# Performance work log

Measured on AMD Instinct MI355X. Metric: run time of the kernel, lower is better.

## Reference

```python
import jax, jax.numpy as jnp
import numpy as np

R = 8          # gate_r
SIGMA = 4.0
PER_SPK_MAX = 32
TOP_M = 64
N_HEADS = 8


def _window_mean(A, spikes, r):
    # A:[B,T], spikes:[B,S] int -> mean of A over [ti-r, ti+r] clipped to [0,T)
    B, T = A.shape
    off = jnp.arange(-r, r + 1)
    t = spikes[:, :, None] + off                      # [B,S,W]
    valid = (t >= 0) & (t < T)
    tc = jnp.clip(t, 0, T - 1)
    vals = A[jnp.arange(B)[:, None, None], tc]        # [B,S,W]
    return (vals * valid).sum(-1) / jnp.maximum(valid.sum(-1), 1)


def setup_inputs() -> dict:
    key = jax.random.key(0)
    ks = jax.random.split(key, 12)
    Kspk, B, T, S0 = 3, 8, 8192, 128
    d_proj = d_c = d_model = 512
    s = 0.02
    return {
        'proj_feats': jax.random.normal(ks[0], (B, T, d_proj), jnp.float32),
        'h_ctc': jax.random.normal(ks[1], (Kspk, B, T, d_c), jnp.float32),
        'A': jax.random.uniform(ks[2], (Kspk, B, T), jnp.float32),
        'spikes': jax.random.randint(ks[3], (Kspk, B, S0), 0, T),
        'W_mem': jax.random.normal(ks[4], (d_proj, d_model), jnp.float32) * s,
        'b_mem': jnp.zeros((d_model,), jnp.float32),
        'W_kv': jax.random.normal(ks[5], (Kspk, d_c, 2 * d_model), jnp.float32) * s,
        'b_kv': jnp.zeros((Kspk, 2 * d_model), jnp.float32),
        'W_q': jax.random.normal(ks[6], (d_model, d_model), jnp.float32) * s,
        'b_q': jnp.zeros((d_model,), jnp.float32),
        'W_qkv': jax.random.normal(ks[7], (d_model, 3 * d_model), jnp.float32) * s,
        'b_qkv': jnp.zeros((3 * d_model,), jnp.float32),
        'W_attn_out': jax.random.normal(ks[8], (d_model, d_model), jnp.float32) * s,
        'b_attn_out': jnp.zeros((d_model,), jnp.float32),
        'W_o': jax.random.normal(ks[9], (d_model, d_model), jnp.float32) * s,
        'b_o': jnp.zeros((d_model,), jnp.float32),
    }


def reference(proj_feats, h_ctc, A, spikes, W_mem, b_mem, W_kv, b_kv,
              W_q, b_q, W_qkv, b_qkv, W_attn_out, b_attn_out, W_o, b_o):
    Kspk, B, T, _ = h_ctc.shape
    d_model = W_mem.shape[1]
    hd = d_model // N_HEADS
    # memory = projected mixed features (K = V = M_mem)
    M = proj_feats @ W_mem + b_mem                                  # [B,T,d]
    Wqh, Wkh, Wvh = jnp.split(W_qkv, 3, axis=1)
    bqh, bkh, bvh = jnp.split(b_qkv, 3)
    k_mem = (M @ Wkh + bkh).reshape(B, T, N_HEADS, hd)
    v_mem = (M @ Wvh + bvh).reshape(B, T, N_HEADS, hd)
    off = jnp.arange(-R, R + 1)
    gauss = jnp.exp(-0.5 * (off / SIGMA) ** 2)                      # [W]
    bidx = jnp.arange(B)[:, None, None]
    tracks = []
    for k in range(Kspk):
        A_k, sp = A[k], spikes[k]
        k_keep = min(PER_SPK_MAX, sp.shape[1], TOP_M)
        # prune spikes by local mean of A (top-k per batch)
        sc = jnp.where((sp >= 0) & (sp < T), _window_mean(A_k, sp, R), -1e9)
        _, top_idx = jax.lax.top_k(sc, k_keep)
        spk = jnp.take_along_axis(sp, top_idx, axis=1)              # [B,S]
        # Gaussian-weighted window pooling around each kept spike
        t = spk[:, :, None] + off                                   # [B,S,W]
        valid = (t >= 0) & (t < T)
        tc = jnp.clip(t, 0, T - 1)
        w = gauss * A_k[bidx, tc] * valid                           # [B,S,W]
        Z = jnp.einsum('bsw,bswd->bsd', w, h_ctc[k][bidx, tc]) / (w.sum(-1, keepdims=True) + 1e-6)
        vmask = ((spk >= 0) & (spk < T)).astype(M.dtype)            # all ones here
        # K_seed = first half of kv_ctc[k](Z); queries
        K_seed = (Z @ W_kv[k] + b_kv[k])[..., :d_model]
        Qk = jnp.tanh(K_seed @ W_q + b_q)                           # [B,S,d]
        # cross-attention (nn.MultiheadAttention, batch_first)
        q = (Qk @ Wqh + bqh).reshape(B, -1, N_HEADS, hd)
        attn = jax.nn.softmax(
            jnp.einsum('bqhd,bthd->bhqt', q, k_mem) / jnp.sqrt(jnp.float32(hd)), axis=-1)
        ctx = jnp.einsum('bhqt,bthd->bqhd', attn, v_mem).reshape(B, -1, d_model)
        fused = (ctx @ W_attn_out + b_attn_out) @ W_o + b_o
        # confidence gate (computed under no_grad in the original)
        conf = jax.lax.stop_gradient(jnp.where(vmask > 0, _window_mean(A_k, spk, R), 0.0))
        gk = jax.nn.sigmoid(2.0 * conf) * vmask
        tracks.append(fused * gk[..., None])
    return jnp.concatenate(tracks, axis=1)                          # [B, K*S, d]
```

## Files before the change

kernel.cpp:

```cpp
#include <hip/hip_runtime.h>
#include <hip/hip_bf16.h>


#define T_LEN 8192
#define DMODEL 512
#define NROWS 768

typedef __hip_bfloat16 bf16;
typedef short s16x8 __attribute__((ext_vector_type(8)));
typedef float f32x4 __attribute__((ext_vector_type(4)));
typedef float f4 __attribute__((ext_vector_type(4)));
typedef float f2 __attribute__((ext_vector_type(2)));
typedef int i32x4 __attribute__((ext_vector_type(4)));
typedef struct __attribute__((aligned(16))) { bf16 v[8]; } bf8;

__global__ __launch_bounds__(256) void prep_w2t(const float* __restrict__ Wmem,
                                                const float* __restrict__ Wqkv,
                                                bf16* __restrict__ w2t) {
  __shared__ __align__(16) float As[16][68];
  __shared__ __align__(16) float Bs[16][68];
  int tid = threadIdx.x;
  int j0 = blockIdx.x * 64, i0 = blockIdx.y * 64;
  int ty = tid >> 4, tx = tid & 15;
  float c[4][4];
#pragma unroll
  for (int a = 0; a < 4; a++)
#pragma unroll
    for (int b = 0; b < 4; b++) c[a][b] = 0.f;

  for (int l0 = 0; l0 < 512; l0 += 16) {
    __syncthreads();
    {
      int l = tid >> 4, j4 = (tid & 15) * 4;
      f4 v = *(const f4*)&Wqkv[(size_t)(l0 + l) * 1536 + 512 + j0 + j4];
      *(f4*)&As[l][j4] = v;
    }
    {
      int i = tid >> 2, l4 = (tid & 3) * 4;
      f4 v = *(const f4*)&Wmem[(size_t)(i0 + i) * 512 + l0 + l4];
      Bs[l4 + 0][i] = v[0];
      Bs[l4 + 1][i] = v[1];
      Bs[l4 + 2][i] = v[2];
      Bs[l4 + 3][i] = v[3];
    }
    __syncthreads();
#pragma unroll
    for (int l = 0; l < 16; l++) {
      f4 a = *(f4*)&As[l][ty * 4];
      f4 b = *(f4*)&Bs[l][tx * 4];
#pragma unroll
      for (int jj = 0; jj < 4; jj++)
#pragma unroll
        for (int ii = 0; ii < 4; ii++) c[jj][ii] += a[jj] * b[ii];
    }
  }
#pragma unroll
  for (int jj = 0; jj < 4; jj++)
#pragma unroll
    for (int ii = 0; ii < 4; ii++)
      w2t[(size_t)(j0 + ty * 4 + jj) * 512 + i0 + tx * 4 + ii] =
          __float2bfloat16(c[jj][ii]);
}

__global__ void bias2_kernel(const float* __restrict__ bmem,
                             const float* __restrict__ Wqkv,
                             const float* __restrict__ bqkv,
                             float* __restrict__ b2) {
  int j = blockIdx.x * 256 + threadIdx.x;
  float acc = bqkv[512 + j];
  for (int l = 0; l < 512; l++) acc += bmem[l] * Wqkv[(size_t)l * 1536 + 512 + j];
  b2[j] = acc;
}

__global__ __launch_bounds__(256) void cvt_bf16(const float* __restrict__ x,
                                                bf16* __restrict__ y) {
  int i = blockIdx.x * 256 + threadIdx.x;
  const f4* p = (const f4*)x;
  f4 a = p[(size_t)i * 2], b = p[(size_t)i * 2 + 1];
  __align__(16) bf16 o[8];
  o[0] = __float2bfloat16(a[0]);
  o[1] = __float2bfloat16(a[1]);
  o[2] = __float2bfloat16(a[2]);
  o[3] = __float2bfloat16(a[3]);
  o[4] = __float2bfloat16(b[0]);
  o[5] = __float2bfloat16(b[1]);
  o[6] = __float2bfloat16(b[2]);
  o[7] = __float2bfloat16(b[3]);
  ((f4*)y)[i] = *(f4*)o;
}

__global__ __launch_bounds__(256) void kv_gemm(const bf16* __restrict__ A,
                                               const bf16* __restrict__ Bt,
                                               const float* __restrict__ bias,
                                               bf16* __restrict__ C) {
  __shared__ __align__(16) bf16 As[128 * 32];
  __shared__ __align__(16) bf16 Bs[128 * 32];
  int tid = threadIdx.x;
  int lane = tid & 63, wave = tid >> 6;
  int wm = wave & 1, wn = wave >> 1;
  int m0 = blockIdx.y * 128, n0 = blockIdx.x * 128;
  int l15 = lane & 15, lq = lane >> 4;
  f32x4 acc[4][4];
#pragma unroll
  for (int mi = 0; mi < 4; mi++)
#pragma unroll
    for (int ni = 0; ni < 4; ni++) acc[mi][ni] = (f32x4){0.f, 0.f, 0.f, 0.f};

  for (int k0 = 0; k0 < 512; k0 += 32) {
    __syncthreads();
#pragma unroll
    for (int t = 0; t < 2; t++) {
      int c = t * 256 + tid;
      int row = c >> 2, kq = c & 3;
      s16x8 av = *(const s16x8*)&A[(size_t)(m0 + row) * 512 + k0 + kq * 8];
      s16x8 bv = *(const s16x8*)&Bt[(size_t)(n0 + row) * 512 + k0 + kq * 8];
      *(s16x8*)&As[c * 8] = av;
      *(s16x8*)&Bs[c * 8] = bv;
    }
    __syncthreads();
    s16x8 af[4], bfr[4];
#pragma unroll
    for (int mi = 0; mi < 4; mi++)
      af[mi] = *(s16x8*)&As[(wm * 64 + mi * 16 + l15) * 32 + lq * 8];
#pragma unroll
    for (int ni = 0; ni < 4; ni++)
      bfr[ni] = *(s16x8*)&Bs[(wn * 64 + ni * 16 + l15) * 32 + lq * 8];
#pragma unroll
    for (int mi = 0; mi < 4; mi++)
#pragma unroll
      for (int ni = 0; ni < 4; ni++)
        acc[mi][ni] = __builtin_amdgcn_mfma_f32_16x16x32_bf16(af[mi], bfr[ni],
                                                              acc[mi][ni], 0, 0, 0);
  }
#pragma unroll
  for (int ni = 0; ni < 4; ni++) {
    int col = n0 + wn * 64 + ni * 16 + l15;
    float bcol = bias[col];
#pragma unroll
    for (int mi = 0; mi < 4; mi++) {
      int row = m0 + wm * 64 + mi * 16 + lq * 4;
      f32x4 v = acc[mi][ni];
#pragma unroll
      for (int r = 0; r < 4; r++)
        C[(size_t)(row + r) * 1024 + col] = __float2bfloat16(v[r] + bcol);
    }
  }
}

__global__ __launch_bounds__(128) void topk_kernel(const float* __restrict__ A,
                                                   const int* __restrict__ spikes,
                                                   int* __restrict__ spk_out,
                                                   float* __restrict__ w_out,
                                                   float* __restrict__ winv_out,
                                                   float* __restrict__ gk_out) {
  int kb = blockIdx.x;
  int i = threadIdx.x;
  const float* Ab = A + (size_t)kb * T_LEN;
  __shared__ float s_sc[128];
  __shared__ int s_sp[128];
  __shared__ int s_sel[32];
  int t0 = spikes[kb * 128 + i];
  s_sp[i] = t0;
  float sum = 0.f;
  int cnt = 0;
#pragma unroll
  for (int o = -8; o <= 8; o++) {
    int t = t0 + o;
    if (t >= 0 && t < T_LEN) { sum += Ab[t]; cnt++; }
  }
  float sc = (t0 >= 0 && t0 < T_LEN) ? (sum / (float)max(cnt, 1)) : -1e9f;
  s_sc[i] = sc;
  __syncthreads();
  float sci = s_sc[i];
  int rank = 0;
  for (int j = 0; j < 128; j++) {
    float scj = s_sc[j];
    if (scj > sci || (scj == sci && j < i)) rank++;
  }
  if (rank < 32) s_sel[rank] = i;
  __syncthreads();
  if (i < 32) {
    int sel = s_sel[i];
    int spkv = s_sp[sel];
    float conf = s_sc[sel];
    int r = kb * 32 + i;
    spk_out[r] = spkv;
    bool vmask = (spkv >= 0 && spkv < T_LEN);
    float wsum = 0.f;
#pragma unroll
    for (int o = 0; o < 17; o++) {
      int t = spkv + o - 8;
      bool v = vmask && (t >= 0) && (t < T_LEN);
      int tc = min(max(t, 0), T_LEN - 1);
      float off = (float)(o - 8) * 0.25f;
      float g = expf(-0.5f * off * off);
      float wv = v ? g * Ab[tc] : 0.f;
      wsum += wv;
      w_out[r * 17 + o] = wv;
    }
    winv_out[r] = 1.f / (wsum + 1e-6f);
    gk_out[r] = vmask ? (1.f / (1.f + expf(-2.f * conf))) : 0.f;
  }
}

__global__ __launch_bounds__(256) void z_gather(const float* __restrict__ hctc,
                                                const int* __restrict__ spk,
                                                const float* __restrict__ warr,
                                                const float* __restrict__ winv,
                                                float* __restrict__ Z) {
  int r = blockIdx.x;
  int tid = threadIdx.x;
  int kb = r >> 5;
  const float* h = hctc + (size_t)kb * T_LEN * DMODEL;
  int sp = spk[r];
  float wi = winv[r];
  float acc0 = 0.f, acc1 = 0.f;
#pragma unroll
  for (int o = 0; o < 17; o++) {
    float wv = warr[r * 17 + o];
    int t = min(max(sp + o - 8, 0), T_LEN - 1);
    const float* hp = h + (size_t)t * DMODEL;
    acc0 += wv * hp[tid];
    acc1 += wv * hp[tid + 256];
  }
  Z[(size_t)r * DMODEL + tid] = acc0 * wi;
  Z[(size_t)r * DMODEL + tid + 256] = acc1 * wi;
}

__global__ __launch_bounds__(256) void seed_chain(
    const float* __restrict__ Z, const float* __restrict__ Wkv,
    const float* __restrict__ bkv, const float* __restrict__ Wq,
    const float* __restrict__ bq, const float* __restrict__ Wqkv,
    const float* __restrict__ bqkv, float* __restrict__ qout) {
  __shared__ float Zs[8][512];
  __shared__ float T1[8][512];
  __shared__ float T2[8][512];
  int tid = threadIdx.x;
  int r0 = blockIdx.x * 8;
  int k = r0 >> 8;
  for (int ii = 0; ii < 16; ii++) {
    int idx = tid + ii * 256;
    ((float*)Zs)[idx] = Z[(size_t)r0 * 512 + idx];
  }
  __syncthreads();
  int c0 = tid, c1 = tid + 256;
  {
    const float* W = Wkv + (size_t)k * 512 * 1024;
    float a0[8], a1[8];
#pragma unroll
    for (int i = 0; i < 8; i++) { a0[i] = 0.f; a1[i] = 0.f; }
#pragma unroll 4
    for (int l = 0; l < 512; l++) {
      float w0 = W[(size_t)l * 1024 + c0];
      float w1 = W[(size_t)l * 1024 + c1];
#pragma unroll
      for (int i = 0; i < 8; i++) {
        float z = Zs[i][l];
        a0[i] += z * w0;
        a1[i] += z * w1;
      }
    }
    float bb0 = bkv[k * 1024 + c0], bb1 = bkv[k * 1024 + c1];
#pragma unroll
    for (int i = 0; i < 8; i++) {
      T1[i][c0] = a0[i] + bb0;
      T1[i][c1] = a1[i] + bb1;
    }
  }
  __syncthreads();
  {
    float a0[8], a1[8];
#pragma unroll
    for (int i = 0; i < 8; i++) { a0[i] = 0.f; a1[i] = 0.f; }
#pragma unroll 4
    for (int l = 0; l < 512; l++) {
      float w0 = Wq[(size_t)l * 512 + c0];
      float w1 = Wq[(size_t)l * 512 + c1];
#pragma unroll
      for (int i = 0; i < 8; i++) {
        float z = T1[i][l];
        a0[i] += z * w0;
        a1[i] += z * w1;
      }
    }
    float bb0 = bq[c0], bb1 = bq[c1];
#pragma unroll
    for (int i = 0; i < 8; i++) {
      T2[i][c0] = tanhf(a0[i] + bb0);
      T2[i][c1] = tanhf(a1[i] + bb1);
    }
  }
  __syncthreads();
  {
    float a0[8], a1[8];
#pragma unroll
    for (int i = 0; i < 8; i++) { a0[i] = 0.f; a1[i] = 0.f; }
#pragma unroll 4
    for (int l = 0; l < 512; l++) {
      float w0 = Wqkv[(size_t)l * 1536 + c0];
      float w1 = Wqkv[(size_t)l * 1536 + c1];
#pragma unroll
      for (int i = 0; i < 8; i++) {
        float z = T2[i][l];
        a0[i] += z * w0;
        a1[i] += z * w1;
      }
    }
    float bb0 = bqkv[c0], bb1 = bqkv[c1];
#pragma unroll
    for (int i = 0; i < 8; i++) {
      qout[(size_t)(r0 + i) * 512 + c0] = a0[i] + bb0;
      qout[(size_t)(r0 + i) * 512 + c1] = a1[i] + bb1;
    }
  }
}


static __device__ __forceinline__ unsigned bf16rne(float f) {
  unsigned x = __builtin_bit_cast(unsigned, f);
  return (x + 0x7fffu + ((x >> 16) & 1u)) >> 16;
}
static __device__ __forceinline__ float bfval(unsigned u) {
  return __builtin_bit_cast(float, u << 16);
}
static __device__ __forceinline__ void hilo(float x, unsigned& h, unsigned& l) {
  h = bf16rne(x);
  l = bf16rne(x - bfval(h));
}

__global__ __launch_bounds__(256) void attn_kernel(const bf16* __restrict__ kv,
                                                   const float* __restrict__ qws,
                                                   float* __restrict__ pm,
                                                   float* __restrict__ pl,
                                                   float* __restrict__ pu) {
  __shared__ short Vts[4][2048];
  __shared__ float ctxc[4][32][68];
  __shared__ float cm[4][32];
  __shared__ float cl[4][32];

  int tid = threadIdx.x;
  int w = tid >> 6, lane = tid & 63;
  int l15 = lane & 15, g = lane >> 4;
  int bx = blockIdx.x;
  int c = bx & 7, h = (bx >> 3) & 7, b = (bx >> 6) & 7, k = bx >> 9;
  int kb = k * 8 + b;
  const short* kvS = (const short*)kv;
  int hoff = h * 64;
  int rowK = b * T_LEN + c * 1024 + w * 256;

  s16x8 qf[2][2][2];
#pragma unroll
  for (int qt = 0; qt < 2; qt++)
#pragma unroll
    for (int ds = 0; ds < 2; ds++) {
      const float* qp =
          qws + (size_t)(kb * 32 + qt * 16 + l15) * 512 + hoff + ds * 32 + g * 8;
      f4 x = *(const f4*)qp;
      f4 y = *(const f4*)(qp + 4);
      x *= 0.125f;
      y *= 0.125f;
      s16x8 hi, lo;
#pragma unroll
      for (int j = 0; j < 4; j++) {
        unsigned hb, lb;
        hilo(x[j], hb, lb);
        hi[j] = (short)hb;
        lo[j] = (short)lb;
        hilo(y[j], hb, lb);
        hi[4 + j] = (short)hb;
        lo[4 + j] = (short)lb;
      }
      qf[qt][ds][0] = hi;
      qf[qt][ds][1] = lo;
    }

  float mq[2] = {-3.0e38f, -3.0e38f};
  float lq[2] = {0.f, 0.f};
  f32x4 ctx[4][2];
#pragma unroll
  for (int dt = 0; dt < 4; dt++)
#pragma unroll
    for (int qt = 0; qt < 2; qt++) ctx[dt][qt] = (f32x4){0.f, 0.f, 0.f, 0.f};

  int a0 = (l15 + (((2 * g) & 3) << 4)) << 2;
  int a1 = a0 + 64;

  for (int st = 0; st < 8; st++) {
    int tbase = st * 32;
    s16x8 kf[2][2];
#pragma unroll
    for (int mt = 0; mt < 2; mt++) {
      size_t krow = (size_t)(rowK + tbase + mt * 16 + l15) * 1024 + hoff;
#pragma unroll
      for (int ds = 0; ds < 2; ds++)
        kf[mt][ds] = *(const s16x8*)(kvS + krow + ds * 32 + g * 8);
    }
    s16x8 vv[4];
#pragma unroll
    for (int i = 0; i < 4; i++)
      vv[i] = *(const s16x8*)(kvS +
                              (size_t)(rowK + tbase + i * 8 + (lane >> 3)) * 1024 +
                              512 + hoff + (lane & 7) * 8);
#pragma unroll
    for (int i = 0; i < 4; i++) {
      int kk = i * 8 + (lane >> 3);
      int dbase = (lane & 7) * 8;
#pragma unroll
      for (int j = 0; j < 8; j++) {
        int d = dbase + j;
        Vts[w][d * 32 + (kk & 7) + ((i ^ ((d >> 3) & 3)) << 3)] = vv[i][j];
      }
    }
    s16x8 vfr[4];
#pragma unroll
    for (int dt = 0; dt < 4; dt++) {
      int d = dt * 16 + l15;
      vfr[dt] = *(const s16x8*)&Vts[w][d * 32 + ((g ^ ((d >> 3) & 3)) << 3)];
    }
    f32x4 sa[2][2];
#pragma unroll
    for (int mt = 0; mt < 2; mt++)
#pragma unroll
      for (int qt = 0; qt < 2; qt++) {
        f32x4 acc = (f32x4){0.f, 0.f, 0.f, 0.f};
        acc = __builtin_amdgcn_mfma_f32_16x16x32_bf16(kf[mt][0], qf[qt][0][0], acc, 0, 0, 0);
        acc = __builtin_amdgcn_mfma_f32_16x16x32_bf16(kf[mt][0], qf[qt][0][1], acc, 0, 0, 0);
        acc = __builtin_amdgcn_mfma_f32_16x16x32_bf16(kf[mt][1], qf[qt][1][0], acc, 0, 0, 0);
        acc = __builtin_amdgcn_mfma_f32_16x16x32_bf16(kf[mt][1], qf[qt][1][1], acc, 0, 0, 0);
        sa[mt][qt] = acc;
      }
#pragma unroll
    for (int qt = 0; qt < 2; qt++) {
      f32x4 s0 = sa[0][qt], s1 = sa[1][qt];
      float tm = fmaxf(fmaxf(fmaxf(s0[0], s0[1]), fmaxf(s0[2], s0[3])),
                       fmaxf(fmaxf(s1[0], s1[1]), fmaxf(s1[2], s1[3])));
      tm = fmaxf(tm, __shfl_xor(tm, 16, 64));
      tm = fmaxf(tm, __shfl_xor(tm, 32, 64));
      float mn = fmaxf(mq[qt], tm);
      float p0[4], p1[4];
      float ps = 0.f;
#pragma unroll
      for (int j = 0; j < 4; j++) {
        p0[j] = __expf(s0[j] - mn);
        p1[j] = __expf(s1[j] - mn);
        ps += p0[j] + p1[j];
      }
      ps += __shfl_xor(ps, 16, 64);
      ps += __shfl_xor(ps, 32, 64);
      float sc = __expf(mq[qt] - mn);
      lq[qt] = lq[qt] * sc + ps;
      mq[qt] = mn;
#pragma unroll
      for (int dt = 0; dt < 4; dt++) ctx[dt][qt] *= sc;
      unsigned hh[8], ll[8];
#pragma unroll
      for (int j = 0; j < 4; j++) {
        hilo(p0[j], hh[j], ll[j]);
        hilo(p1[j], hh[4 + j], ll[4 + j]);
      }
      unsigned dh0 = hh[0] | (hh[1] << 16), dh1 = hh[2] | (hh[3] << 16);
      unsigned dh2 = hh[4] | (hh[5] << 16), dh3 = hh[6] | (hh[7] << 16);
      unsigned dl0 = ll[0] | (ll[1] << 16), dl1 = ll[2] | (ll[3] << 16);
      unsigned dl2 = ll[4] | (ll[5] << 16), dl3 = ll[6] | (ll[7] << 16);
      int x0 = __builtin_amdgcn_ds_bpermute(a0, (int)dh0);
      int x1 = __builtin_amdgcn_ds_bpermute(a0, (int)dh1);
      int x2 = __builtin_amdgcn_ds_bpermute(a0, (int)dh2);
      int x3 = __builtin_amdgcn_ds_bpermute(a0, (int)dh3);
      int y0 = __builtin_amdgcn_ds_bpermute(a1, (int)dh0);
      int y1 = __builtin_amdgcn_ds_bpermute(a1, (int)dh1);
      int y2 = __builtin_amdgcn_ds_bpermute(a1, (int)dh2);
      int y3 = __builtin_amdgcn_ds_bpermute(a1, (int)dh3);
      i32x4 fh;
      if (g < 2)
        fh = (i32x4){x0, x1, y0, y1};
      else
        fh = (i32x4){x2, x3, y2, y3};
      x0 = __builtin_amdgcn_ds_bpermute(a0, (int)dl0);
      x1 = __builtin_amdgcn_ds_bpermute(a0, (int)dl1);
      x2 = __builtin_amdgcn_ds_bpermute(a0, (int)dl2);
      x3 = __builtin_amdgcn_ds_bpermute(a0, (int)dl3);
      y0 = __builtin_amdgcn_ds_bpermute(a1, (int)dl0);
      y1 = __builtin_amdgcn_ds_bpermute(a1, (int)dl1);
      y2 = __builtin_amdgcn_ds_bpermute(a1, (int)dl2);
      y3 = __builtin_amdgcn_ds_bpermute(a1, (int)dl3);
      i32x4 fl;
      if (g < 2)
        fl = (i32x4){x0, x1, y0, y1};
      else
        fl = (i32x4){x2, x3, y2, y3};
      s16x8 pfh = __builtin_bit_cast(s16x8, fh);
      s16x8 pfl = __builtin_bit_cast(s16x8, fl);
#pragma unroll
      for (int dt = 0; dt < 4; dt++) {
        ctx[dt][qt] =
            __builtin_amdgcn_mfma_f32_16x16x32_bf16(vfr[dt], pfh, ctx[dt][qt], 0, 0, 0);
        ctx[dt][qt] =
            __builtin_amdgcn_mfma_f32_16x16x32_bf16(vfr[dt], pfl, ctx[dt][qt], 0, 0, 0);
      }
    }
  }

  if (g == 0) {
#pragma unroll
    for (int qt = 0; qt < 2; qt++) {
      cm[w][qt * 16 + l15] = mq[qt];
      cl[w][qt * 16 + l15] = lq[qt];
    }
  }
#pragma unroll
  for (int dt = 0; dt < 4; dt++)
#pragma unroll
    for (int qt = 0; qt < 2; qt++) {
      f32x4 v = ctx[dt][qt];
      int q = qt * 16 + l15;
      int dd = dt * 16 + g * 4;
#pragma unroll
      for (int r = 0; r < 4; r++) ctxc[w][q][dd + r] = v[r];
    }
  __syncthreads();

  {
    int q = tid >> 3, dg = tid & 7;
    float m0 = cm[0][q], m1 = cm[1][q], m2 = cm[2][q], m3 = cm[3][q];
    float ms = fmaxf(fmaxf(m0, m1), fmaxf(m2, m3));
    float e0 = __expf(m0 - ms), e1 = __expf(m1 - ms);
    float e2 = __expf(m2 - ms), e3 = __expf(m3 - ms);
    float ls = e0 * cl[0][q] + e1 * cl[1][q] + e2 * cl[2][q] + e3 * cl[3][q];
    int pbase = (((k * 8 + b) * 8 + h) * 8 + c) * 32;
    size_t urow = (size_t)(pbase + q) * 64 + dg * 8;
#pragma unroll
    for (int half = 0; half < 2; half++) {
      int d0 = dg * 8 + half * 4;
      f4 acc = e0 * *(const f4*)&ctxc[0][q][d0] + e1 * *(const f4*)&ctxc[1][q][d0] +
               e2 * *(const f4*)&ctxc[2][q][d0] + e3 * *(const f4*)&ctxc[3][q][d0];
      *(f4*)&pu[urow + half * 4] = acc;
    }
    if (dg == 0) {
      pm[pbase + q] = ms;
      pl[pbase + q] = ls;
    }
  }
}

__global__ __launch_bounds__(256) void out_chain(
    const float* __restrict__ pm, const float* __restrict__ pl,
    const float* __restrict__ pu, const float* __restrict__ Watt,
    const float* __restrict__ batt, const float* __restrict__ Wo,
    const float* __restrict__ bo, const float* __restrict__ gk,
    float* __restrict__ out) {
  __shared__ float Cs[8][512];
  __shared__ float T1[8][512];
  int tid = threadIdx.x;
  int r0 = blockIdx.x * 8;
  {
    int ri = tid >> 5, hh = (tid >> 2) & 7, dq = tid & 3;
    int d0 = dq * 16;
    int r = r0 + ri;
    int k = r >> 8, b = (r >> 5) & 7, s = r & 31;
    int pb0 = ((((k * 8 + b) * 8 + hh) * 8) * 32) + s;
    float mstar = -3.0e38f;
#pragma unroll
    for (int cc = 0; cc < 8; cc++) mstar = fmaxf(mstar, pm[pb0 + cc * 32]);
    float ls = 0.f;
    f4 us[4];
#pragma unroll
    for (int t4 = 0; t4 < 4; t4++) us[t4] = (f4){0.f, 0.f, 0.f, 0.f};
#pragma unroll
    for (int cc = 0; cc < 8; cc++) {
      int pidx = pb0 + cc * 32;
      float wv = __expf(pm[pidx] - mstar);
      ls += wv * pl[pidx];
      const f4* up = (const f4*)&pu[(size_t)pidx * 64 + d0];
#pragma unroll
      for (int t4 = 0; t4 < 4; t4++) us[t4] += up[t4] * wv;
    }
    float inv = 1.f / ls;
#pragma unroll
    for (int t4 = 0; t4 < 4; t4++)
#pragma unroll
      for (int j = 0; j < 4; j++) Cs[ri][hh * 64 + d0 + t4 * 4 + j] = us[t4][j] * inv;
  }
  __syncthreads();
  int c0 = tid, c1 = tid + 256;
  {
    float a0[8], a1[8];
#pragma unroll
    for (int i = 0; i < 8; i++) { a0[i] = 0.f; a1[i] = 0.f; }
#pragma unroll 4
    for (int l = 0; l < 512; l++) {
      float w0 = Watt[(size_t)l * 512 + c0];
      float w1 = Watt[(size_t)l * 512 + c1];
#pragma unroll
      for (int i = 0; i < 8; i++) {
        float z = Cs[i][l];
        a0[i] += z * w0;
        a1[i] += z * w1;
      }
    }
    float bb0 = batt[c0], bb1 = batt[c1];
#pragma unroll
    for (int i = 0; i < 8; i++) {
      T1[i][c0] = a0[i] + bb0;
      T1[i][c1] = a1[i] + bb1;
    }
  }
  __syncthreads();
  {
    float a0[8], a1[8];
#pragma unroll
    for (int i = 0; i < 8; i++) { a0[i] = 0.f; a1[i] = 0.f; }
#pragma unroll 4
    for (int l = 0; l < 512; l++) {
      float w0 = Wo[(size_t)l * 512 + c0];
      float w1 = Wo[(size_t)l * 512 + c1];
#pragma unroll
      for (int i = 0; i < 8; i++) {
        float z = T1[i][l];
        a0[i] += z * w0;
        a1[i] += z * w1;
      }
    }
    float bb0 = bo[c0], bb1 = bo[c1];
#pragma unroll
    for (int i = 0; i < 8; i++) {
      int r = r0 + i;
      int k = r >> 8, b = (r >> 5) & 7, s = r & 31;
      float g = gk[r];
      size_t orow = (size_t)(b * 96 + k * 32 + s) * 512;
      out[orow + c0] = (a0[i] + bb0) * g;
      out[orow + c1] = (a1[i] + bb1) * g;
    }
  }
}

extern "C" void kernel_launch(void* const* d_in, const int* in_sizes, int n_in,
                              void* d_out, int out_size, void* d_ws, size_t ws_size,
                              hipStream_t stream) {
  const float* proj = (const float*)d_in[0];
  const float* hctc = (const float*)d_in[1];
  const float* A = (const float*)d_in[2];
  const int* spikes = (const int*)d_in[3];
  const float* Wmem = (const float*)d_in[4];
  const float* bmem = (const float*)d_in[5];
  const float* Wkv = (const float*)d_in[6];
  const float* bkv = (const float*)d_in[7];
  const float* Wq = (const float*)d_in[8];
  const float* bq = (const float*)d_in[9];
  const float* Wqkv = (const float*)d_in[10];
  const float* bqkv = (const float*)d_in[11];
  const float* Watt = (const float*)d_in[12];
  const float* batt = (const float*)d_in[13];
  const float* Wo = (const float*)d_in[14];
  const float* bo = (const float*)d_in[15];
  float* out = (float*)d_out;
  (void)in_sizes; (void)n_in; (void)out_size; (void)ws_size;

  char* w = (char*)d_ws;
  bf16* projb = (bf16*)(w + 0);
  bf16* kvb   = (bf16*)(w + 67108864);
  bf16* w2t   = (bf16*)(w + 201326592);
  float* b2   = (float*)(w + 202375168);
  int* spk    = (int*)(w + 202379264);
  float* warr = (float*)(w + 202382336);
  float* winv = (float*)(w + 202434560);
  float* gk   = (float*)(w + 202437632);
  float* Zb   = (float*)(w + 202440704);
  float* qws  = (float*)(w + 204013568);
  float* pm   = (float*)(w + 205586432);
  float* pl   = (float*)(w + 205783040);
  float* pu   = (float*)(w + 205979648);

  prep_w2t<<<dim3(16, 8), 256, 0, stream>>>(Wmem, Wqkv, w2t);
  bias2_kernel<<<4, 256, 0, stream>>>(bmem, Wqkv, bqkv, b2);
  cvt_bf16<<<16384, 256, 0, stream>>>(proj, projb);
  kv_gemm<<<dim3(8, 512), 256, 0, stream>>>(projb, w2t, b2, kvb);
  topk_kernel<<<24, 128, 0, stream>>>(A, spikes, spk, warr, winv, gk);
  z_gather<<<768, 256, 0, stream>>>(hctc, spk, warr, winv, Zb);
  seed_chain<<<96, 256, 0, stream>>>(Zb, Wkv, bkv, Wq, bq, Wqkv, bqkv, qws);
  attn_kernel<<<1536, 256, 0, stream>>>(kvb, qws, pm, pl, pu);
  out_chain<<<96, 256, 0, stream>>>(pm, pl, pu, Watt, batt, Wo, bo, gk, out);
}
```

Measured before the change: 1.152 ms.

## Share K/V tiles across speakers in attention, async LDS loads and coalesced GEMM epilogue

The attention kernel now handles all three speaker query sets in one block. Each K/V tile is loaded and transposed once and reused for three sets of queries, which cuts K/V memory traffic and the grid size by three. The queries for all speakers are staged through LDS, and the online-softmax state is kept per speaker in registers. The kv_gemm now uses global_load_lds direct-to-LDS loads, swaps the MFMA operands, and writes its output through an LDS-staged, coalesced 16-byte store. The bias2 reduction is also split over more threads. The costs are much higher register pressure in attention (three sets of accumulators) and fewer blocks to fill the GPU.

```diff
diff --git a/kernel.cpp b/kernel.cpp
--- a/kernel.cpp
+++ b/kernel.cpp
@@ -8,11 +8,14 @@
 
 typedef __hip_bfloat16 bf16;
 typedef short s16x8 __attribute__((ext_vector_type(8)));
+typedef short s16x4 __attribute__((ext_vector_type(4)));
 typedef float f32x4 __attribute__((ext_vector_type(4)));
 typedef float f4 __attribute__((ext_vector_type(4)));
 typedef float f2 __attribute__((ext_vector_type(2)));
 typedef int i32x4 __attribute__((ext_vector_type(4)));
-typedef struct __attribute__((aligned(16))) { bf16 v[8]; } bf8;
+
+typedef __attribute__((address_space(3))) void* lds_vp;
+typedef const __attribute__((address_space(1))) void* gbl_cvp;
 
 __global__ __launch_bounds__(256) void prep_w2t(const float* __restrict__ Wmem,
                                                 const float* __restrict__ Wqkv,
@@ -62,14 +65,23 @@
           __float2bfloat16(c[jj][ii]);
 }
 
-__global__ void bias2_kernel(const float* __restrict__ bmem,
-                             const float* __restrict__ Wqkv,
-                             const float* __restrict__ bqkv,
-                             float* __restrict__ b2) {
-  int j = blockIdx.x * 256 + threadIdx.x;
-  float acc = bqkv[512 + j];
-  for (int l = 0; l < 512; l++) acc += bmem[l] * Wqkv[(size_t)l * 1536 + 512 + j];
-  b2[j] = acc;
+__global__ __launch_bounds__(256) void bias2_kernel(const float* __restrict__ bmem,
+                                                    const float* __restrict__ Wqkv,
+                                                    const float* __restrict__ bqkv,
+                                                    float* __restrict__ b2) {
+  __shared__ float red[4][64];
+  int j0 = blockIdx.x * 64;
+  int jc = threadIdx.x & 63, lp = threadIdx.x >> 6;
+  int j = j0 + jc;
+  float acc = 0.f;
+  for (int l = lp * 128; l < lp * 128 + 128; l++)
+    acc += bmem[l] * Wqkv[(size_t)l * 1536 + 512 + j];
+  red[lp][jc] = acc;
+  __syncthreads();
+  if (threadIdx.x < 64) {
+    float s = red[0][jc] + red[1][jc] + red[2][jc] + red[3][jc];
+    b2[j0 + jc] = s + bqkv[512 + j0 + jc];
+  }
 }
 
 __global__ __launch_bounds__(256) void cvt_bf16(const float* __restrict__ x,
@@ -93,56 +105,73 @@
                                                const bf16* __restrict__ Bt,
                                                const float* __restrict__ bias,
                                                bf16* __restrict__ C) {
-  __shared__ __align__(16) bf16 As[128 * 32];
-  __shared__ __align__(16) bf16 Bs[128 * 32];
+  __shared__ __align__(16) char sm[16384];
+  bf16* As = (bf16*)sm;
+  bf16* Bs = (bf16*)(sm + 8192);
   int tid = threadIdx.x;
   int lane = tid & 63, wave = tid >> 6;
   int wm = wave & 1, wn = wave >> 1;
   int m0 = blockIdx.y * 128, n0 = blockIdx.x * 128;
-  int l15 = lane & 15, lq = lane >> 4;
+  int l15 = lane & 15, g = lane >> 4;
   f32x4 acc[4][4];
 #pragma unroll
   for (int mi = 0; mi < 4; mi++)
 #pragma unroll
     for (int ni = 0; ni < 4; ni++) acc[mi][ni] = (f32x4){0.f, 0.f, 0.f, 0.f};
 
+  int arow = tid >> 2, akq = (tid & 3) * 8;
   for (int k0 = 0; k0 < 512; k0 += 32) {
     __syncthreads();
 #pragma unroll
-    for (int t = 0; t < 2; t++) {
-      int c = t * 256 + tid;
-      int row = c >> 2, kq = c & 3;
-      s16x8 av = *(const s16x8*)&A[(size_t)(m0 + row) * 512 + k0 + kq * 8];
-      s16x8 bv = *(const s16x8*)&Bt[(size_t)(n0 + row) * 512 + k0 + kq * 8];
-      *(s16x8*)&As[c * 8] = av;
-      *(s16x8*)&Bs[c * 8] = bv;
+    for (int i = 0; i < 2; i++) {
+      const bf16* ga = &A[(size_t)(m0 + i * 64 + arow) * 512 + k0 + akq];
+      const bf16* gb = &Bt[(size_t)(n0 + i * 64 + arow) * 512 + k0 + akq];
+      __builtin_amdgcn_global_load_lds((gbl_cvp)ga,
+                                       (lds_vp)(sm + (i * 256 + wave * 64) * 16),
+                                       16, 0, 0);
+      __builtin_amdgcn_global_load_lds((gbl_cvp)gb,
+                                       (lds_vp)(sm + 8192 + (i * 256 + wave * 64) * 16),
+                                       16, 0, 0);
     }
     __syncthreads();
     s16x8 af[4], bfr[4];
 #pragma unroll
     for (int mi = 0; mi < 4; mi++)
-      af[mi] = *(s16x8*)&As[(wm * 64 + mi * 16 + l15) * 32 + lq * 8];
+      af[mi] = *(s16x8*)&As[(wm * 64 + mi * 16 + l15) * 32 + g * 8];
 #pragma unroll
     for (int ni = 0; ni < 4; ni++)
-      bfr[ni] = *(s16x8*)&Bs[(wn * 64 + ni * 16 + l15) * 32 + lq * 8];
+      bfr[ni] = *(s16x8*)&Bs[(wn * 64 + ni * 16 + l15) * 32 + g * 8];
 #pragma unroll
     for (int mi = 0; mi < 4; mi++)
 #pragma unroll
       for (int ni = 0; ni < 4; ni++)
-        acc[mi][ni] = __builtin_amdgcn_mfma_f32_16x16x32_bf16(af[mi], bfr[ni],
+        acc[mi][ni] = __builtin_amdgcn_mfma_f32_16x16x32_bf16(bfr[ni], af[mi],
                                                               acc[mi][ni], 0, 0, 0);
   }
-#pragma unroll
-  for (int ni = 0; ni < 4; ni++) {
-    int col = n0 + wn * 64 + ni * 16 + l15;
-    float bcol = bias[col];
-#pragma unroll
-    for (int mi = 0; mi < 4; mi++) {
-      int row = m0 + wm * 64 + mi * 16 + lq * 4;
+
+  short* ep = (short*)sm;
+  int band = wm * 16 + l15;
+#pragma unroll
+  for (int mi = 0; mi < 4; mi++) {
+    __syncthreads();
+#pragma unroll
+    for (int ni = 0; ni < 4; ni++) {
+      int c0 = wn * 64 + ni * 16 + g * 4;
+      f4 bv = *(const f4*)&bias[n0 + c0];
       f32x4 v = acc[mi][ni];
-#pragma unroll
-      for (int r = 0; r < 4; r++)
-        C[(size_t)(row + r) * 1024 + col] = __float2bfloat16(v[r] + bcol);
+      __align__(8) bf16 pk[4];
+#pragma unroll
+      for (int r = 0; r < 4; r++) pk[r] = __float2bfloat16(v[r] + bv[r]);
+      *(s16x4*)&ep[band * 136 + c0] = *(s16x4*)pk;
+    }
+    __syncthreads();
+#pragma unroll
+    for (int it = 0; it < 2; it++) {
+      int cidx = it * 256 + tid;
+      int brow = cidx >> 4, ch = cidx & 15;
+      s16x8 val = *(s16x8*)&ep[brow * 136 + ch * 8];
+      int row = m0 + (brow >> 4) * 64 + mi * 16 + (brow & 15);
+      *(s16x8*)&C[(size_t)row * 1024 + n0 + ch * 8] = val;
     }
   }
 }
@@ -333,54 +362,66 @@
                                                    float* __restrict__ pm,
                                                    float* __restrict__ pl,
                                                    float* __restrict__ pu) {
-  __shared__ short Vts[4][2048];
-  __shared__ float ctxc[4][32][68];
-  __shared__ float cm[4][32];
-  __shared__ float cl[4][32];
+  __shared__ __align__(16) char smem[40960];
+  short* Vts = (short*)smem;
+  short* Qls = (short*)(smem + 16384);
+  float* ctxc = (float*)smem;
+  float* cmS = (float*)(smem + 34816);
+  float* clS = (float*)(smem + 35328);
 
   int tid = threadIdx.x;
   int w = tid >> 6, lane = tid & 63;
   int l15 = lane & 15, g = lane >> 4;
   int bx = blockIdx.x;
-  int c = bx & 7, h = (bx >> 3) & 7, b = (bx >> 6) & 7, k = bx >> 9;
-  int kb = k * 8 + b;
+  int c = bx & 7, h = (bx >> 3) & 7, b = bx >> 6;
   const short* kvS = (const short*)kv;
   int hoff = h * 64;
   int rowK = b * T_LEN + c * 1024 + w * 256;
 
-  s16x8 qf[2][2][2];
-#pragma unroll
-  for (int qt = 0; qt < 2; qt++)
-#pragma unroll
-    for (int ds = 0; ds < 2; ds++) {
-      const float* qp =
-          qws + (size_t)(kb * 32 + qt * 16 + l15) * 512 + hoff + ds * 32 + g * 8;
-      f4 x = *(const f4*)qp;
-      f4 y = *(const f4*)(qp + 4);
-      x *= 0.125f;
-      y *= 0.125f;
-      s16x8 hi, lo;
-#pragma unroll
-      for (int j = 0; j < 4; j++) {
-        unsigned hb, lb;
-        hilo(x[j], hb, lb);
-        hi[j] = (short)hb;
-        lo[j] = (short)lb;
-        hilo(y[j], hb, lb);
-        hi[4 + j] = (short)hb;
-        lo[4 + j] = (short)lb;
-      }
-      qf[qt][ds][0] = hi;
-      qf[qt][ds][1] = lo;
-    }
-
-  float mq[2] = {-3.0e38f, -3.0e38f};
-  float lq[2] = {0.f, 0.f};
-  f32x4 ctx[4][2];
-#pragma unroll
-  for (int dt = 0; dt < 4; dt++)
-#pragma unroll
-    for (int qt = 0; qt < 2; qt++) ctx[dt][qt] = (f32x4){0.f, 0.f, 0.f, 0.f};
+#pragma unroll
+  for (int p = 0; p < 3; p++) {
+    int slot = p * 4 + (tid >> 6);
+    int kk = slot >> 2, qt = (slot >> 1) & 1, ds = slot & 1;
+    int ln = tid & 63;
+    int sl15 = ln & 15, sg = ln >> 4;
+    const float* qp = qws + (size_t)((kk * 8 + b) * 32 + qt * 16 + sl15) * 512 +
+                      hoff + ds * 32 + sg * 8;
+    f4 x = *(const f4*)qp;
+    f4 y = *(const f4*)(qp + 4);
+    x *= 0.125f;
+    y *= 0.125f;
+    s16x8 hi, lo;
+#pragma unroll
+    for (int j = 0; j < 4; j++) {
+      unsigned hb, lb;
+      hilo(x[j], hb, lb);
+      hi[j] = (short)hb;
+      lo[j] = (short)lb;
+      hilo(y[j], hb, lb);
+      hi[4 + j] = (short)hb;
+      lo[4 + j] = (short)lb;
+    }
+    *(s16x8*)&Qls[((slot * 2 + 0) * 64 + ln) * 8] = hi;
+    *(s16x8*)&Qls[((slot * 2 + 1) * 64 + ln) * 8] = lo;
+  }
+  __syncthreads();
+
+  float mq[3][2];
+  float lsm[3][2];
+  f32x4 ctx[3][4][2];
+#pragma unroll
+  for (int kk = 0; kk < 3; kk++)
+#pragma unroll
+    for (int qt = 0; qt < 2; qt++) {
+      mq[kk][qt] = -3.0e38f;
+      lsm[kk][qt] = 0.f;
+    }
+#pragma unroll
+  for (int kk = 0; kk < 3; kk++)
+#pragma unroll
+    for (int dt = 0; dt < 4; dt++)
+#pragma unroll
+      for (int qt = 0; qt < 2; qt++) ctx[kk][dt][qt] = (f32x4){0.f, 0.f, 0.f, 0.f};
 
   int a0 = (l15 + (((2 * g) & 3) << 4)) << 2;
   int a1 = a0 + 64;
@@ -395,149 +436,168 @@
       for (int ds = 0; ds < 2; ds++)
         kf[mt][ds] = *(const s16x8*)(kvS + krow + ds * 32 + g * 8);
     }
-    s16x8 vv[4];
-#pragma unroll
-    for (int i = 0; i < 4; i++)
-      vv[i] = *(const s16x8*)(kvS +
-                              (size_t)(rowK + tbase + i * 8 + (lane >> 3)) * 1024 +
-                              512 + hoff + (lane & 7) * 8);
-#pragma unroll
-    for (int i = 0; i < 4; i++) {
-      int kk = i * 8 + (lane >> 3);
-      int dbase = (lane & 7) * 8;
-#pragma unroll
-      for (int j = 0; j < 8; j++) {
-        int d = dbase + j;
-        Vts[w][d * 32 + (kk & 7) + ((i ^ ((d >> 3) & 3)) << 3)] = vv[i][j];
+    {
+      s16x8 vv[4];
+#pragma unroll
+      for (int i = 0; i < 4; i++)
+        vv[i] = *(const s16x8*)(kvS +
+                                (size_t)(rowK + tbase + i * 8 + (lane >> 3)) * 1024 +
+                                512 + hoff + (lane & 7) * 8);
+#pragma unroll
+      for (int i = 0; i < 4; i++) {
+        int tk = i * 8 + (lane >> 3);
+        int dbase = (lane & 7) * 8;
+#pragma unroll
+        for (int j = 0; j < 8; j++) {
+          int d = dbase + j;
+          Vts[w * 2048 + d * 32 + (tk & 7) + ((i ^ ((d >> 3) & 3)) << 3)] = vv[i][j];
+        }
       }
     }
     s16x8 vfr[4];
 #pragma unroll
     for (int dt = 0; dt < 4; dt++) {
       int d = dt * 16 + l15;
-      vfr[dt] = *(const s16x8*)&Vts[w][d * 32 + ((g ^ ((d >> 3) & 3)) << 3)];
-    }
-    f32x4 sa[2][2];
-#pragma unroll
-    for (int mt = 0; mt < 2; mt++)
+      vfr[dt] = *(const s16x8*)&Vts[w * 2048 + d * 32 + ((g ^ ((d >> 3) & 3)) << 3)];
+    }
+#pragma unroll
+    for (int kk = 0; kk < 3; kk++) {
+      s16x8 qf[2][2][2];
+#pragma unroll
+      for (int qt = 0; qt < 2; qt++)
+#pragma unroll
+        for (int ds = 0; ds < 2; ds++)
+#pragma unroll
+          for (int hl = 0; hl < 2; hl++)
+            qf[qt][ds][hl] =
+                *(const s16x8*)&Qls[(((kk * 4 + qt * 2 + ds) * 2 + hl) * 64 + lane) * 8];
+      f32x4 sa[2][2];
+#pragma unroll
+      for (int mt = 0; mt < 2; mt++)
+#pragma unroll
+        for (int qt = 0; qt < 2; qt++) {
+          f32x4 acc = (f32x4){0.f, 0.f, 0.f, 0.f};
+          acc = __builtin_amdgcn_mfma_f32_16x16x32_bf16(kf[mt][0], qf[qt][0][0], acc, 0, 0, 0);
+          acc = __builtin_amdgcn_mfma_f32_16x16x32_bf16(kf[mt][0], qf[qt][0][1], acc, 0, 0, 0);
+          acc = __builtin_amdgcn_mfma_f32_16x16x32_bf16(kf[mt][1], qf[qt][1][0], acc, 0, 0, 0);
+          acc = __builtin_amdgcn_mfma_f32_16x16x32_bf16(kf[mt][1], qf[qt][1][1], acc, 0, 0, 0);
+          sa[mt][qt] = acc;
+        }
 #pragma unroll
       for (int qt = 0; qt < 2; qt++) {
-        f32x4 acc = (f32x4){0.f, 0.f, 0.f, 0.f};
-        acc = __builtin_amdgcn_mfma_f32_16x16x32_bf16(kf[mt][0], qf[qt][0][0], acc, 0, 0, 0);
-        acc = __builtin_amdgcn_mfma_f32_16x16x32_bf16(kf[mt][0], qf[qt][0][1], acc, 0, 0, 0);
-        acc = __builtin_amdgcn_mfma_f32_16x16x32_bf16(kf[mt][1], qf[qt][1][0], acc, 0, 0, 0);
-        acc = __builtin_amdgcn_mfma_f32_16x16x32_bf16(kf[mt][1], qf[qt][1][1], acc, 0, 0, 0);
-        sa[mt][qt] = acc;
-      }
-#pragma unroll
-    for (int qt = 0; qt < 2; qt++) {
-      f32x4 s0 = sa[0][qt], s1 = sa[1][qt];
-      float tm = fmaxf(fmaxf(fmaxf(s0[0], s0[1]), fmaxf(s0[2], s0[3])),
-                       fmaxf(fmaxf(s1[0], s1[1]), fmaxf(s1[2], s1[3])));
-      tm = fmaxf(tm, __shfl_xor(tm, 16, 64));
-      tm = fmaxf(tm, __shfl_xor(tm, 32, 64));
-      float mn = fmaxf(mq[qt], tm);
-      float p0[4], p1[4];
-      float ps = 0.f;
-#pragma unroll
-      for (int j = 0; j < 4; j++) {
-        p0[j] = __expf(s0[j] - mn);
-        p1[j] = __expf(s1[j] - mn);
-        ps += p0[j] + p1[j];
-      }
-      ps += __shfl_xor(ps, 16, 64);
-      ps += __shfl_xor(ps, 32, 64);
-      float sc = __expf(mq[qt] - mn);
-      lq[qt] = lq[qt] * sc + ps;
-      mq[qt] = mn;
-#pragma unroll
-      for (int dt = 0; dt < 4; dt++) ctx[dt][qt] *= sc;
-      unsigned hh[8], ll[8];
-#pragma unroll
-      for (int j = 0; j < 4; j++) {
-        hilo(p0[j], hh[j], ll[j]);
-        hilo(p1[j], hh[4 + j], ll[4 + j]);
-      }
-      unsigned dh0 = hh[0] | (hh[1] << 16), dh1 = hh[2] | (hh[3] << 16);
-      unsigned dh2 = hh[4] | (hh[5] << 16), dh3 = hh[6] | (hh[7] << 16);
-      unsigned dl0 = ll[0] | (ll[1] << 16), dl1 = ll[2] | (ll[3] << 16);
-      unsigned dl2 = ll[4] | (ll[5] << 16), dl3 = ll[6] | (ll[7] << 16);
-      int x0 = __builtin_amdgcn_ds_bpermute(a0, (int)dh0);
-      int x1 = __builtin_amdgcn_ds_bpermute(a0, (int)dh1);
-      int x2 = __builtin_amdgcn_ds_bpermute(a0, (int)dh2);
-      int x3 = __builtin_amdgcn_ds_bpermute(a0, (int)dh3);
-      int y0 = __builtin_amdgcn_ds_bpermute(a1, (int)dh0);
-      int y1 = __builtin_amdgcn_ds_bpermute(a1, (int)dh1);
-      int y2 = __builtin_amdgcn_ds_bpermute(a1, (int)dh2);
-      int y3 = __builtin_amdgcn_ds_bpermute(a1, (int)dh3);
-      i32x4 fh;
-      if (g < 2)
-        fh = (i32x4){x0, x1, y0, y1};
-      else
-        fh = (i32x4){x2, x3, y2, y3};
-      x0 = __builtin_amdgcn_ds_bpermute(a0, (int)dl0);
-      x1 = __builtin_amdgcn_ds_bpermute(a0, (int)dl1);
-      x2 = __builtin_amdgcn_ds_bpermute(a0, (int)dl2);
-      x3 = __builtin_amdgcn_ds_bpermute(a0, (int)dl3);
-      y0 = __builtin_amdgcn_ds_bpermute(a1, (int)dl0);
-      y1 = __builtin_amdgcn_ds_bpermute(a1, (int)dl1);
-      y2 = __builtin_amdgcn_ds_bpermute(a1, (int)dl2);
-      y3 = __builtin_amdgcn_ds_bpermute(a1, (int)dl3);
-      i32x4 fl;
-      if (g < 2)
-        fl = (i32x4){x0, x1, y0, y1};
-      else
-        fl = (i32x4){x2, x3, y2, y3};
-      s16x8 pfh = __builtin_bit_cast(s16x8, fh);
-      s16x8 pfl = __builtin_bit_cast(s16x8, fl);
-#pragma unroll
-      for (int dt = 0; dt < 4; dt++) {
-        ctx[dt][qt] =
-            __builtin_amdgcn_mfma_f32_16x16x32_bf16(vfr[dt], pfh, ctx[dt][qt], 0, 0, 0);
-        ctx[dt][qt] =
-            __builtin_amdgcn_mfma_f32_16x16x32_bf16(vfr[dt], pfl, ctx[dt][qt], 0, 0, 0);
-      }
-    }
-  }
-
-  if (g == 0) {
-#pragma unroll
-    for (int qt = 0; qt < 2; qt++) {
-      cm[w][qt * 16 + l15] = mq[qt];
-      cl[w][qt * 16 + l15] = lq[qt];
-    }
-  }
-#pragma unroll
-  for (int dt = 0; dt < 4; dt++)
-#pragma unroll
-    for (int qt = 0; qt < 2; qt++) {
-      f32x4 v = ctx[dt][qt];
-      int q = qt * 16 + l15;
-      int dd = dt * 16 + g * 4;
-#pragma unroll
-      for (int r = 0; r < 4; r++) ctxc[w][q][dd + r] = v[r];
-    }
-  __syncthreads();
-
-  {
-    int q = tid >> 3, dg = tid & 7;
-    float m0 = cm[0][q], m1 = cm[1][q], m2 = cm[2][q], m3 = cm[3][q];
-    float ms = fmaxf(fmaxf(m0, m1), fmaxf(m2, m3));
-    float e0 = __expf(m0 - ms), e1 = __expf(m1 - ms);
-    float e2 = __expf(m2 - ms), e3 = __expf(m3 - ms);
-    float ls = e0 * cl[0][q] + e1 * cl[1][q] + e2 * cl[2][q] + e3 * cl[3][q];
-    int pbase = (((k * 8 + b) * 8 + h) * 8 + c) * 32;
-    size_t urow = (size_t)(pbase + q) * 64 + dg * 8;
-#pragma unroll
-    for (int half = 0; half < 2; half++) {
-      int d0 = dg * 8 + half * 4;
-      f4 acc = e0 * *(const f4*)&ctxc[0][q][d0] + e1 * *(const f4*)&ctxc[1][q][d0] +
-               e2 * *(const f4*)&ctxc[2][q][d0] + e3 * *(const f4*)&ctxc[3][q][d0];
-      *(f4*)&pu[urow + half * 4] = acc;
-    }
-    if (dg == 0) {
-      pm[pbase + q] = ms;
-      pl[pbase + q] = ls;
+        f32x4 s0 = sa[0][qt], s1 = sa[1][qt];
+        float tm = fmaxf(fmaxf(fmaxf(s0[0], s0[1]), fmaxf(s0[2], s0[3])),
+                         fmaxf(fmaxf(s1[0], s1[1]), fmaxf(s1[2], s1[3])));
+        tm = fmaxf(tm, __shfl_xor(tm, 16, 64));
+        tm = fmaxf(tm, __shfl_xor(tm, 32, 64));
+        float mn = fmaxf(mq[kk][qt], tm);
+        float p0[4], p1[4];
+        float ps = 0.f;
+#pragma unroll
+        for (int j = 0; j < 4; j++) {
+          p0[j] = __expf(s0[j] - mn);
+          p1[j] = __expf(s1[j] - mn);
+          ps += p0[j] + p1[j];
+        }
+        ps += __shfl_xor(ps, 16, 64);
+        ps += __shfl_xor(ps, 32, 64);
+        float sc = __expf(mq[kk][qt] - mn);
+        lsm[kk][qt] = lsm[kk][qt] * sc + ps;
+        mq[kk][qt] = mn;
+#pragma unroll
+        for (int dt = 0; dt < 4; dt++) ctx[kk][dt][qt] *= sc;
+        unsigned hh[8], ll[8];
+#pragma unroll
+        for (int j = 0; j < 4; j++) {
+          hilo(p0[j], hh[j], ll[j]);
+          hilo(p1[j], hh[4 + j], ll[4 + j]);
+        }
+        unsigned dh0 = hh[0] | (hh[1] << 16), dh1 = hh[2] | (hh[3] << 16);
+        unsigned dh2 = hh[4] | (hh[5] << 16), dh3 = hh[6] | (hh[7] << 16);
+        unsigned dl0 = ll[0] | (ll[1] << 16), dl1 = ll[2] | (ll[3] << 16);
+        unsigned dl2 = ll[4] | (ll[5] << 16), dl3 = ll[6] | (ll[7] << 16);
+        int x0 = __builtin_amdgcn_ds_bpermute(a0, (int)dh0);
+        int x1 = __builtin_amdgcn_ds_bpermute(a0, (int)dh1);
+        int x2 = __builtin_amdgcn_ds_bpermute(a0, (int)dh2);
+        int x3 = __builtin_amdgcn_ds_bpermute(a0, (int)dh3);
+        int y0 = __builtin_amdgcn_ds_bpermute(a1, (int)dh0);
+        int y1 = __builtin_amdgcn_ds_bpermute(a1, (int)dh1);
+        int y2 = __builtin_amdgcn_ds_bpermute(a1, (int)dh2);
+        int y3 = __builtin_amdgcn_ds_bpermute(a1, (int)dh3);
+        i32x4 fh;
+        if (g < 2)
+          fh = (i32x4){x0, x1, y0, y1};
+        else
+          fh = (i32x4){x2, x3, y2, y3};
+        x0 = __builtin_amdgcn_ds_bpermute(a0, (int)dl0);
+        x1 = __builtin_amdgcn_ds_bpermute(a0, (int)dl1);
+        x2 = __builtin_amdgcn_ds_bpermute(a0, (int)dl2);
+        x3 = __builtin_amdgcn_ds_bpermute(a0, (int)dl3);
+        y0 = __builtin_amdgcn_ds_bpermute(a1, (int)dl0);
+        y1 = __builtin_amdgcn_ds_bpermute(a1, (int)dl1);
+        y2 = __builtin_amdgcn_ds_bpermute(a1, (int)dl2);
+        y3 = __builtin_amdgcn_ds_bpermute(a1, (int)dl3);
+        i32x4 fl;
+        if (g < 2)
+          fl = (i32x4){x0, x1, y0, y1};
+        else
+          fl = (i32x4){x2, x3, y2, y3};
+        s16x8 pfh = __builtin_bit_cast(s16x8, fh);
+        s16x8 pfl = __builtin_bit_cast(s16x8, fl);
+#pragma unroll
+        for (int dt = 0; dt < 4; dt++) {
+          ctx[kk][dt][qt] =
+              __builtin_amdgcn_mfma_f32_16x16x32_bf16(vfr[dt], pfh, ctx[kk][dt][qt], 0, 0, 0);
+          ctx[kk][dt][qt] =
+              __builtin_amdgcn_mfma_f32_16x16x32_bf16(vfr[dt], pfl, ctx[kk][dt][qt], 0, 0, 0);
+        }
+      }
+    }
+  }
+
+#pragma unroll
+  for (int kk = 0; kk < 3; kk++) {
+    __syncthreads();
+    if (g == 0) {
+#pragma unroll
+      for (int qt = 0; qt < 2; qt++) {
+        cmS[w * 32 + qt * 16 + l15] = mq[kk][qt];
+        clS[w * 32 + qt * 16 + l15] = lsm[kk][qt];
+      }
+    }
+#pragma unroll
+    for (int dt = 0; dt < 4; dt++)
+#pragma unroll
+      for (int qt = 0; qt < 2; qt++) {
+        f32x4 v = ctx[kk][dt][qt];
+        int q = qt * 16 + l15;
+        int dd = dt * 16 + g * 4;
+#pragma unroll
+        for (int r = 0; r < 4; r++) ctxc[(w * 32 + q) * 68 + dd + r] = v[r];
+      }
+    __syncthreads();
+    {
+      int q = tid >> 3, dg = tid & 7;
+      float m0 = cmS[q], m1 = cmS[32 + q], m2 = cmS[64 + q], m3 = cmS[96 + q];
+      float ms = fmaxf(fmaxf(m0, m1), fmaxf(m2, m3));
+      float e0 = __expf(m0 - ms), e1 = __expf(m1 - ms);
+      float e2 = __expf(m2 - ms), e3 = __expf(m3 - ms);
+      float ls = e0 * clS[q] + e1 * clS[32 + q] + e2 * clS[64 + q] + e3 * clS[96 + q];
+      int pbase = (((kk * 8 + b) * 8 + h) * 8 + c) * 32;
+      size_t urow = (size_t)(pbase + q) * 64 + dg * 8;
+#pragma unroll
+      for (int half = 0; half < 2; half++) {
+        int d0 = dg * 8 + half * 4;
+        f4 acc = e0 * *(const f4*)&ctxc[q * 68 + d0] +
+                 e1 * *(const f4*)&ctxc[(32 + q) * 68 + d0] +
+                 e2 * *(const f4*)&ctxc[(64 + q) * 68 + d0] +
+                 e3 * *(const f4*)&ctxc[(96 + q) * 68 + d0];
+        *(f4*)&pu[urow + half * 4] = acc;
+      }
+      if (dg == 0) {
+        pm[pbase + q] = ms;
+        pl[pbase + q] = ls;
+      }
     }
   }
 }
@@ -671,12 +731,12 @@
   float* pu   = (float*)(w + 205979648);
 
   prep_w2t<<<dim3(16, 8), 256, 0, stream>>>(Wmem, Wqkv, w2t);
-  bias2_kernel<<<4, 256, 0, stream>>>(bmem, Wqkv, bqkv, b2);
+  bias2_kernel<<<16, 256, 0, stream>>>(bmem, Wqkv, bqkv, b2);
   cvt_bf16<<<16384, 256, 0, stream>>>(proj, projb);
   kv_gemm<<<dim3(8, 512), 256, 0, stream>>>(projb, w2t, b2, kvb);
   topk_kernel<<<24, 128, 0, stream>>>(A, spikes, spk, warr, winv, gk);
   z_gather<<<768, 256, 0, stream>>>(hctc, spk, warr, winv, Zb);
   seed_chain<<<96, 256, 0, stream>>>(Zb, Wkv, bkv, Wq, bq, Wqkv, bqkv, qws);
-  attn_kernel<<<1536, 256, 0, stream>>>(kvb, qws, pm, pl, pu);
+  attn_kernel<<<512, 256, 0, stream>>>(kvb, qws, pm, pl, pu);
   out_chain<<<96, 256, 0, stream>>>(pm, pl, pu, Watt, batt, Wo, bo, gk, out);
 }
```

Measured after the change: 1.125 ms. 2.3% less time.
